# Kernel tuning notes

Measured on AMD Instinct MI355X. Metric: run time of the kernel, lower is better.

Reference implementation:

```python
import jax, jax.numpy as jnp
import numpy as np

H = 4096          # hidden_size
I = 2048          # moe_intermediate_size * n_shared_experts
SWIGLU_LIMIT = 10.0
QMAX = 127.0


def _quantize_weight(w):
    # per-output-channel symmetric int8 quantization of a float weight [out, in]
    s = jnp.maximum(jnp.max(jnp.abs(w), axis=1) / QMAX, 1e-8)      # [out]
    q = jnp.clip(jnp.round(w / s[:, None]), -QMAX, QMAX)           # int8-valued
    return q.astype(jnp.float32), s.astype(jnp.float32)


def setup_inputs() -> dict:
    key = jax.random.key(0)
    ks = jax.random.split(key, 4)
    x = jax.random.normal(ks[0], (2, 4096, H), dtype=jnp.float32)
    w_gate, s_wgate = _quantize_weight(jax.random.normal(ks[1], (I, H)) * 0.02)
    w_up, s_wup = _quantize_weight(jax.random.normal(ks[2], (I, H)) * 0.02)
    w_down, s_wdown = _quantize_weight(jax.random.normal(ks[3], (H, I)) * 0.02)
    inv_gate = jnp.ones((H,), jnp.float32)
    inv_up = jnp.ones((H,), jnp.float32)
    inv_inter = jnp.ones((I,), jnp.float32)
    return {"x": x, "w_gate": w_gate, "s_wgate": s_wgate, "w_up": w_up,
            "s_wup": s_wup, "w_down": w_down, "s_wdown": s_wdown,
            "inv_gate": inv_gate, "inv_up": inv_up, "inv_inter": inv_inter}


def _dynamic_quant(x, inv_smooth):
    # per-token symmetric int8 dynamic quant with smoothing scale
    xs = x.astype(jnp.float32) * inv_smooth                        # [T, D]
    scale = jnp.maximum(jnp.max(jnp.abs(xs), axis=-1, keepdims=True) / QMAX, 1e-8)
    q = jnp.clip(jnp.round(xs / scale), -QMAX, QMAX)
    return q, scale


def _quant_gemm(q, x_scale, w_q, w_scale):
    acc = q @ w_q.T                                                # fp32 accumulate
    return acc * x_scale * w_scale[None, :]


def reference(x, w_gate, s_wgate, w_up, s_wup, w_down, s_wdown,
              inv_gate, inv_up, inv_inter):
    orig_shape = x.shape
    x_flat = x.reshape(-1, H).astype(jnp.bfloat16)                 # [T, H]
    qg, sg = _dynamic_quant(x_flat, inv_gate)
    qu, su = _dynamic_quant(x_flat, inv_up)
    gate_out = _quant_gemm(qg, sg, w_gate, s_wgate)                # [T, I]
    up_out = _quant_gemm(qu, su, w_up, s_wup)                      # [T, I]
    inter = jax.nn.silu(gate_out) * up_out
    inter = jnp.clip(inter, -SWIGLU_LIMIT, SWIGLU_LIMIT).astype(jnp.bfloat16)
    qi, si = _dynamic_quant(inter, inv_inter)
    out = _quant_gemm(qi, si, w_down, s_wdown)                     # [T, H]
    return out.reshape(orig_shape)
```

## Files before the change

kernel.cpp:

```cpp
#include <hip/hip_runtime.h>
#include <hip/hip_bf16.h>


typedef __attribute__((ext_vector_type(4))) int i32x4;

__device__ __forceinline__ void async16(void* lds, const void* g) {
  __builtin_amdgcn_global_load_lds(
      (const __attribute__((address_space(1))) void*)g,
      (__attribute__((address_space(3))) void*)lds, 16, 0, 0);
}

__device__ __forceinline__ i32x4 mfma_i8(i32x4 a, i32x4 b, i32x4 c) {
  return __builtin_amdgcn_mfma_i32_16x16x64_i8(a, b, c, 0, 0, 0);
}

__device__ __forceinline__ float bf16_rne_f(float f) {
  unsigned u = __float_as_uint(f);
  u += 0x7fffu + ((u >> 16) & 1u);
  return __uint_as_float(u & 0xffff0000u);
}

__device__ __forceinline__ unsigned short bf16_bits(float f) {
  unsigned u = __float_as_uint(f);
  u += 0x7fffu + ((u >> 16) & 1u);
  return (unsigned short)(u >> 16);
}

__device__ __forceinline__ float bf16_to_f(unsigned short h) {
  return __uint_as_float(((unsigned)h) << 16);
}

#define BARRIER __builtin_amdgcn_s_barrier()
#define LGKM0 asm volatile("s_waitcnt lgkmcnt(0)" ::: "memory")
#define WAIT_VM8 asm volatile("s_waitcnt vmcnt(8)" ::: "memory")
#define WAIT_VM4 asm volatile("s_waitcnt vmcnt(4)" ::: "memory")
#define WAIT_VM0 asm volatile("s_waitcnt vmcnt(0)" ::: "memory")

__global__ void wconv_kernel(const float* __restrict__ w,
                             signed char* __restrict__ wq, int n) {
  int i = (blockIdx.x * 256 + threadIdx.x) * 4;
  if (i >= n) return;
  float4 f = *(const float4*)(w + i);
  signed char c[4] __attribute__((aligned(4)));
  c[0] = (signed char)(int)rintf(f.x);
  c[1] = (signed char)(int)rintf(f.y);
  c[2] = (signed char)(int)rintf(f.z);
  c[3] = (signed char)(int)rintf(f.w);
  *(int*)(wq + i) = *(const int*)c;
}

__global__ __launch_bounds__(256) void quant_x_kernel(
    const float* __restrict__ x, const float* __restrict__ invg,
    const float* __restrict__ invu, signed char* __restrict__ qg,
    signed char* __restrict__ qu, float* __restrict__ sg,
    float* __restrict__ su, int H) {
  const int t = blockIdx.x, tid = threadIdx.x;
  const float* xr = x + (size_t)t * H;
  const int c0 = tid * 16;
  float xg[16], xu[16];
  float mg = 0.f, mu = 0.f;
#pragma unroll
  for (int v = 0; v < 4; ++v) {
    float4 f = *(const float4*)(xr + c0 + v * 4);
    float4 ig = *(const float4*)(invg + c0 + v * 4);
    float4 iu = *(const float4*)(invu + c0 + v * 4);
    float b0 = bf16_rne_f(f.x), b1 = bf16_rne_f(f.y);
    float b2 = bf16_rne_f(f.z), b3 = bf16_rne_f(f.w);
    xg[v * 4 + 0] = b0 * ig.x; xg[v * 4 + 1] = b1 * ig.y;
    xg[v * 4 + 2] = b2 * ig.z; xg[v * 4 + 3] = b3 * ig.w;
    xu[v * 4 + 0] = b0 * iu.x; xu[v * 4 + 1] = b1 * iu.y;
    xu[v * 4 + 2] = b2 * iu.z; xu[v * 4 + 3] = b3 * iu.w;
#pragma unroll
    for (int j = 0; j < 4; ++j) {
      mg = fmaxf(mg, fabsf(xg[v * 4 + j]));
      mu = fmaxf(mu, fabsf(xu[v * 4 + j]));
    }
  }
#pragma unroll
  for (int off = 32; off > 0; off >>= 1) {
    mg = fmaxf(mg, __shfl_xor(mg, off));
    mu = fmaxf(mu, __shfl_xor(mu, off));
  }
  __shared__ float smg[4], smu[4];
  if ((tid & 63) == 0) { smg[tid >> 6] = mg; smu[tid >> 6] = mu; }
  __syncthreads();
  mg = fmaxf(fmaxf(smg[0], smg[1]), fmaxf(smg[2], smg[3]));
  mu = fmaxf(fmaxf(smu[0], smu[1]), fmaxf(smu[2], smu[3]));
  const float scg = fmaxf(mg / 127.0f, 1e-8f);
  const float scu = fmaxf(mu / 127.0f, 1e-8f);
  signed char og[16] __attribute__((aligned(16)));
  signed char ou[16] __attribute__((aligned(16)));
#pragma unroll
  for (int j = 0; j < 16; ++j) {
    og[j] = (signed char)(int)fminf(fmaxf(rintf(xg[j] / scg), -127.f), 127.f);
    ou[j] = (signed char)(int)fminf(fmaxf(rintf(xu[j] / scu), -127.f), 127.f);
  }
  *(i32x4*)(qg + (size_t)t * H + c0) = *(const i32x4*)og;
  *(i32x4*)(qu + (size_t)t * H + c0) = *(const i32x4*)ou;
  if (tid == 0) { sg[t] = scg; su[t] = scu; }
}

#define G1_STAGE(b, kk)                                                       \
  {                                                                           \
    _Pragma("unroll") for (int p = 0; p < 2; ++p) {                           \
      const int g_ = p * 256 + tid;                                           \
      const int r_ = g_ >> 2;                                                 \
      const int c_ = (g_ & 3) ^ ((r_ >> 1) & 3);                              \
      const size_t ga_ = (size_t)(row0 + r_) * H + (kk) + c_ * 16;            \
      const size_t gb_ = (size_t)(col0 + r_) * H + (kk) + c_ * 16;            \
      async16(&Ag[b][g_ * 16], qg + ga_);                                     \
      async16(&Au[b][g_ * 16], qu + ga_);                                     \
      async16(&Bg[b][g_ * 16], wg + gb_);                                     \
      async16(&Bu[b][g_ * 16], wu + gb_);                                     \
    }                                                                         \
  }

__global__ __launch_bounds__(256, 2) void gemm1_kernel(
    const signed char* __restrict__ qg, const signed char* __restrict__ qu,
    const float* __restrict__ sg, const float* __restrict__ su,
    const signed char* __restrict__ wg, const signed char* __restrict__ wu,
    const float* __restrict__ swg, const float* __restrict__ swu,
    unsigned short* __restrict__ inter, int H, int I) {
  __shared__ signed char Ag[2][128 * 64] __attribute__((aligned(16)));
  __shared__ signed char Au[2][128 * 64] __attribute__((aligned(16)));
  __shared__ signed char Bg[2][128 * 64] __attribute__((aligned(16)));
  __shared__ signed char Bu[2][128 * 64] __attribute__((aligned(16)));
  const int tid = threadIdx.x;
  const int lane = tid & 63, wave = tid >> 6;
  const int row0 = blockIdx.x * 128, col0 = blockIdx.y * 128;
  const int wm = (wave & 1) * 64, wn = (wave >> 1) * 64;
  const int mrow = lane & 15, quad = lane >> 4;
  const int NT = H >> 6;

  int offA[4], offB[4];
#pragma unroll
  for (int i = 0; i < 4; ++i) {
    const int ra = wm + i * 16 + mrow;
    offA[i] = ra * 64 + ((quad ^ ((ra >> 1) & 3)) << 4);
    const int rb = wn + i * 16 + mrow;
    offB[i] = rb * 64 + ((quad ^ ((rb >> 1) & 3)) << 4);
  }

  i32x4 accG[4][4], accU[4][4];
#pragma unroll
  for (int i = 0; i < 4; ++i)
#pragma unroll
    for (int j = 0; j < 4; ++j) {
      accG[i][j] = i32x4{0, 0, 0, 0};
      accU[i][j] = i32x4{0, 0, 0, 0};
    }

  G1_STAGE(0, 0);

  int cur = 0;
  for (int kt = 0; kt < NT; ++kt) {
    if (kt + 1 < NT) {
      G1_STAGE(cur ^ 1, (kt + 1) << 6);
      WAIT_VM8;
    } else {
      WAIT_VM0;
    }
    BARRIER;

    i32x4 aG[4], aU[4], bG[4], bU[4];
#pragma unroll
    for (int i = 0; i < 4; ++i) {
      aG[i] = *(const i32x4*)(&Ag[cur][0] + offA[i]);
      aU[i] = *(const i32x4*)(&Au[cur][0] + offA[i]);
      bG[i] = *(const i32x4*)(&Bg[cur][0] + offB[i]);
      bU[i] = *(const i32x4*)(&Bu[cur][0] + offB[i]);
    }
#pragma unroll
    for (int i = 0; i < 4; ++i)
#pragma unroll
      for (int j = 0; j < 4; ++j) {
        accG[i][j] = mfma_i8(aG[i], bG[j], accG[i][j]);
        accU[i][j] = mfma_i8(aU[i], bU[j], accU[i][j]);
      }

    LGKM0;
    BARRIER;
    cur ^= 1;
  }

  float swgc[4], swuc[4];
#pragma unroll
  for (int j = 0; j < 4; ++j) {
    const int c = col0 + wn + j * 16 + mrow;
    swgc[j] = swg[c];
    swuc[j] = swu[c];
  }
#pragma unroll
  for (int i = 0; i < 4; ++i) {
#pragma unroll
    for (int r = 0; r < 4; ++r) {
      const int row = row0 + wm + i * 16 + quad * 4 + r;
      const float sgr = sg[row], sur = su[row];
#pragma unroll
      for (int j = 0; j < 4; ++j) {
        const int c = col0 + wn + j * 16 + mrow;
        const float g = (float)accG[i][j][r] * sgr * swgc[j];
        const float u = (float)accU[i][j][r] * sur * swuc[j];
        const float sig = 1.f / (1.f + expf(-g));
        float v = (g * sig) * u;
        v = fminf(fmaxf(v, -10.f), 10.f);
        inter[(size_t)row * I + c] = bf16_bits(v);
      }
    }
  }
}

__global__ __launch_bounds__(256) void quant_i_kernel(
    const unsigned short* __restrict__ inter, const float* __restrict__ invi,
    signed char* __restrict__ qi, float* __restrict__ si, int I) {
  const int t = blockIdx.x, tid = threadIdx.x;
  const unsigned short* ir = inter + (size_t)t * I;
  const int c0 = tid * 8;
  uint4 pk = *(const uint4*)(ir + c0);
  float4 i0 = *(const float4*)(invi + c0);
  float4 i1 = *(const float4*)(invi + c0 + 4);
  float xs[8];
  xs[0] = bf16_to_f(pk.x & 0xffffu) * i0.x;
  xs[1] = bf16_to_f(pk.x >> 16) * i0.y;
  xs[2] = bf16_to_f(pk.y & 0xffffu) * i0.z;
  xs[3] = bf16_to_f(pk.y >> 16) * i0.w;
  xs[4] = bf16_to_f(pk.z & 0xffffu) * i1.x;
  xs[5] = bf16_to_f(pk.z >> 16) * i1.y;
  xs[6] = bf16_to_f(pk.w & 0xffffu) * i1.z;
  xs[7] = bf16_to_f(pk.w >> 16) * i1.w;
  float m = 0.f;
#pragma unroll
  for (int j = 0; j < 8; ++j) m = fmaxf(m, fabsf(xs[j]));
#pragma unroll
  for (int off = 32; off > 0; off >>= 1) m = fmaxf(m, __shfl_xor(m, off));
  __shared__ float sm[4];
  if ((tid & 63) == 0) sm[tid >> 6] = m;
  __syncthreads();
  m = fmaxf(fmaxf(sm[0], sm[1]), fmaxf(sm[2], sm[3]));
  const float s = fmaxf(m / 127.0f, 1e-8f);
  signed char o[8] __attribute__((aligned(8)));
#pragma unroll
  for (int j = 0; j < 8; ++j)
    o[j] = (signed char)(int)fminf(fmaxf(rintf(xs[j] / s), -127.f), 127.f);
  *(unsigned long long*)(qi + (size_t)t * I + c0) = *(const unsigned long long*)o;
  if (tid == 0) si[t] = s;
}

#define G2_STAGE(b, kk)                                                       \
  {                                                                           \
    _Pragma("unroll") for (int p = 0; p < 2; ++p) {                           \
      const int g_ = p * 256 + tid;                                           \
      const int r_ = g_ >> 2;                                                 \
      const int c_ = (g_ & 3) ^ ((r_ >> 1) & 3);                              \
      async16(&As[b][g_ * 16],                                                \
              qi + (size_t)(row0 + r_) * I + (kk) + c_ * 16);                 \
      async16(&Bs[b][g_ * 16],                                                \
              wd + (size_t)(col0 + r_) * I + (kk) + c_ * 16);                 \
    }                                                                         \
  }

__global__ __launch_bounds__(256, 2) void gemm2_kernel(
    const signed char* __restrict__ qi, const float* __restrict__ si,
    const signed char* __restrict__ wd, const float* __restrict__ swd,
    float* __restrict__ out, int H, int I) {
  __shared__ signed char As[2][128 * 64] __attribute__((aligned(16)));
  __shared__ signed char Bs[2][128 * 64] __attribute__((aligned(16)));
  const int tid = threadIdx.x;
  const int lane = tid & 63, wave = tid >> 6;
  const int row0 = blockIdx.x * 128, col0 = blockIdx.y * 128;
  const int wm = (wave & 1) * 64, wn = (wave >> 1) * 64;
  const int mrow = lane & 15, quad = lane >> 4;
  const int NT = I >> 6;

  int offA[4], offB[4];
#pragma unroll
  for (int i = 0; i < 4; ++i) {
    const int ra = wm + i * 16 + mrow;
    offA[i] = ra * 64 + ((quad ^ ((ra >> 1) & 3)) << 4);
    const int rb = wn + i * 16 + mrow;
    offB[i] = rb * 64 + ((quad ^ ((rb >> 1) & 3)) << 4);
  }

  i32x4 acc[4][4];
#pragma unroll
  for (int i = 0; i < 4; ++i)
#pragma unroll
    for (int j = 0; j < 4; ++j) acc[i][j] = i32x4{0, 0, 0, 0};

  G2_STAGE(0, 0);

  int cur = 0;
  for (int kt = 0; kt < NT; ++kt) {
    if (kt + 1 < NT) {
      G2_STAGE(cur ^ 1, (kt + 1) << 6);
      WAIT_VM4;
    } else {
      WAIT_VM0;
    }
    BARRIER;

    i32x4 a[4], b[4];
#pragma unroll
    for (int i = 0; i < 4; ++i) {
      a[i] = *(const i32x4*)(&As[cur][0] + offA[i]);
      b[i] = *(const i32x4*)(&Bs[cur][0] + offB[i]);
    }
#pragma unroll
    for (int i = 0; i < 4; ++i)
#pragma unroll
      for (int j = 0; j < 4; ++j) acc[i][j] = mfma_i8(a[i], b[j], acc[i][j]);

    LGKM0;
    BARRIER;
    cur ^= 1;
  }

  float swc[4];
#pragma unroll
  for (int j = 0; j < 4; ++j) swc[j] = swd[col0 + wn + j * 16 + mrow];
#pragma unroll
  for (int i = 0; i < 4; ++i) {
#pragma unroll
    for (int r = 0; r < 4; ++r) {
      const int row = row0 + wm + i * 16 + quad * 4 + r;
      const float sir = si[row];
#pragma unroll
      for (int j = 0; j < 4; ++j) {
        const int c = col0 + wn + j * 16 + mrow;
        out[(size_t)row * H + c] = (float)acc[i][j][r] * sir * swc[j];
      }
    }
  }
}

extern "C" void kernel_launch(void* const* d_in, const int* in_sizes, int n_in,
                              void* d_out, int out_size, void* d_ws,
                              size_t ws_size, hipStream_t stream) {
  const float* x = (const float*)d_in[0];
  const float* w_gate = (const float*)d_in[1];
  const float* s_wgate = (const float*)d_in[2];
  const float* w_up = (const float*)d_in[3];
  const float* s_wup = (const float*)d_in[4];
  const float* w_down = (const float*)d_in[5];
  const float* s_wdown = (const float*)d_in[6];
  const float* inv_gate = (const float*)d_in[7];
  const float* inv_up = (const float*)d_in[8];
  const float* inv_inter = (const float*)d_in[9];
  float* out = (float*)d_out;

  const int H = in_sizes[6];
  const int I = in_sizes[2];
  const int T = in_sizes[0] / H;

  char* ws = (char*)d_ws;
  size_t off = 0;
  signed char* wqg = (signed char*)(ws + off); off += (size_t)I * H;
  signed char* wqu = (signed char*)(ws + off); off += (size_t)I * H;
  signed char* wqd = (signed char*)(ws + off); off += (size_t)H * I;
  signed char* qg  = (signed char*)(ws + off); off += (size_t)T * H;
  signed char* qu  = (signed char*)(ws + off); off += (size_t)T * H;
  unsigned short* inter = (unsigned short*)(ws + off); off += (size_t)T * I * 2;
  float* sg = (float*)(ws + off); off += (size_t)T * 4;
  float* su = (float*)(ws + off); off += (size_t)T * 4;
  float* si = (float*)(ws + off); off += (size_t)T * 4;
  signed char* qi = qg;

  const int nW = I * H;
  wconv_kernel<<<nW / 1024, 256, 0, stream>>>(w_gate, wqg, nW);
  wconv_kernel<<<nW / 1024, 256, 0, stream>>>(w_up, wqu, nW);
  wconv_kernel<<<nW / 1024, 256, 0, stream>>>(w_down, wqd, nW);

  quant_x_kernel<<<T, 256, 0, stream>>>(x, inv_gate, inv_up, qg, qu, sg, su, H);

  dim3 g1(T / 128, I / 128);
  gemm1_kernel<<<g1, 256, 0, stream>>>(qg, qu, sg, su, wqg, wqu, s_wgate,
                                       s_wup, inter, H, I);

  quant_i_kernel<<<T, 256, 0, stream>>>(inter, inv_inter, qi, si, I);

  dim3 g2(T / 128, H / 128);
  gemm2_kernel<<<g2, 256, 0, stream>>>(qi, si, wqd, s_wdown, out, H, I);
}
```

Before: 612.1 us.

## Load weight operands directly from global into registers, bypassing LDS

Both GEMM kernels stop staging the weight (B) tiles through shared memory and instead have each lane read its B fragments straight from global memory into registers at the start of every K-step. Only the activation tiles still go through double-buffered LDS, and the vmcnt waits are lowered to match the smaller async load count. This halves LDS footprint and LDS traffic and may allow higher occupancy. In exchange, weight tiles are re-read per wave from global/L2 without sharing across waves in the block, and the loads are issued in the same iteration they are consumed, so their latency is exposed rather than prefetched.

```diff
diff --git a/kernel.cpp b/kernel.cpp
--- a/kernel.cpp
+++ b/kernel.cpp
@@ -32,8 +32,8 @@
 
 #define BARRIER __builtin_amdgcn_s_barrier()
 #define LGKM0 asm volatile("s_waitcnt lgkmcnt(0)" ::: "memory")
-#define WAIT_VM8 asm volatile("s_waitcnt vmcnt(8)" ::: "memory")
 #define WAIT_VM4 asm volatile("s_waitcnt vmcnt(4)" ::: "memory")
+#define WAIT_VM2 asm volatile("s_waitcnt vmcnt(2)" ::: "memory")
 #define WAIT_VM0 asm volatile("s_waitcnt vmcnt(0)" ::: "memory")
 
 __global__ void wconv_kernel(const float* __restrict__ w,
@@ -107,11 +107,8 @@
       const int r_ = g_ >> 2;                                                 \
       const int c_ = (g_ & 3) ^ ((r_ >> 1) & 3);                              \
       const size_t ga_ = (size_t)(row0 + r_) * H + (kk) + c_ * 16;            \
-      const size_t gb_ = (size_t)(col0 + r_) * H + (kk) + c_ * 16;            \
       async16(&Ag[b][g_ * 16], qg + ga_);                                     \
       async16(&Au[b][g_ * 16], qu + ga_);                                     \
-      async16(&Bg[b][g_ * 16], wg + gb_);                                     \
-      async16(&Bu[b][g_ * 16], wu + gb_);                                     \
     }                                                                         \
   }
 
@@ -123,8 +120,6 @@
     unsigned short* __restrict__ inter, int H, int I) {
   __shared__ signed char Ag[2][128 * 64] __attribute__((aligned(16)));
   __shared__ signed char Au[2][128 * 64] __attribute__((aligned(16)));
-  __shared__ signed char Bg[2][128 * 64] __attribute__((aligned(16)));
-  __shared__ signed char Bu[2][128 * 64] __attribute__((aligned(16)));
   const int tid = threadIdx.x;
   const int lane = tid & 63, wave = tid >> 6;
   const int row0 = blockIdx.x * 128, col0 = blockIdx.y * 128;
@@ -132,14 +127,15 @@
   const int mrow = lane & 15, quad = lane >> 4;
   const int NT = H >> 6;
 
-  int offA[4], offB[4];
+  int offA[4];
 #pragma unroll
   for (int i = 0; i < 4; ++i) {
     const int ra = wm + i * 16 + mrow;
     offA[i] = ra * 64 + ((quad ^ ((ra >> 1) & 3)) << 4);
-    const int rb = wn + i * 16 + mrow;
-    offB[i] = rb * 64 + ((quad ^ ((rb >> 1) & 3)) << 4);
-  }
+  }
+  const size_t jstep = (size_t)16 * H;
+  const signed char* wgB = wg + (size_t)(col0 + wn + mrow) * H + quad * 16;
+  const signed char* wuB = wu + (size_t)(col0 + wn + mrow) * H + quad * 16;
 
   i32x4 accG[4][4], accU[4][4];
 #pragma unroll
@@ -154,21 +150,28 @@
 
   int cur = 0;
   for (int kt = 0; kt < NT; ++kt) {
+    const int kk = kt << 6;
+
+    i32x4 bG[4], bU[4];
+#pragma unroll
+    for (int j = 0; j < 4; ++j) {
+      bG[j] = *(const i32x4*)(wgB + (size_t)j * jstep + kk);
+      bU[j] = *(const i32x4*)(wuB + (size_t)j * jstep + kk);
+    }
+
     if (kt + 1 < NT) {
-      G1_STAGE(cur ^ 1, (kt + 1) << 6);
-      WAIT_VM8;
+      G1_STAGE(cur ^ 1, kk + 64);
+      WAIT_VM4;
     } else {
       WAIT_VM0;
     }
     BARRIER;
 
-    i32x4 aG[4], aU[4], bG[4], bU[4];
+    i32x4 aG[4], aU[4];
 #pragma unroll
     for (int i = 0; i < 4; ++i) {
       aG[i] = *(const i32x4*)(&Ag[cur][0] + offA[i]);
       aU[i] = *(const i32x4*)(&Au[cur][0] + offA[i]);
-      bG[i] = *(const i32x4*)(&Bg[cur][0] + offB[i]);
-      bU[i] = *(const i32x4*)(&Bu[cur][0] + offB[i]);
     }
 #pragma unroll
     for (int i = 0; i < 4; ++i)
@@ -254,8 +257,6 @@
       const int c_ = (g_ & 3) ^ ((r_ >> 1) & 3);                              \
       async16(&As[b][g_ * 16],                                                \
               qi + (size_t)(row0 + r_) * I + (kk) + c_ * 16);                 \
-      async16(&Bs[b][g_ * 16],                                                \
-              wd + (size_t)(col0 + r_) * I + (kk) + c_ * 16);                 \
     }                                                                         \
   }
 
@@ -264,7 +265,6 @@
     const signed char* __restrict__ wd, const float* __restrict__ swd,
     float* __restrict__ out, int H, int I) {
   __shared__ signed char As[2][128 * 64] __attribute__((aligned(16)));
-  __shared__ signed char Bs[2][128 * 64] __attribute__((aligned(16)));
   const int tid = threadIdx.x;
   const int lane = tid & 63, wave = tid >> 6;
   const int row0 = blockIdx.x * 128, col0 = blockIdx.y * 128;
@@ -272,14 +272,14 @@
   const int mrow = lane & 15, quad = lane >> 4;
   const int NT = I >> 6;
 
-  int offA[4], offB[4];
+  int offA[4];
 #pragma unroll
   for (int i = 0; i < 4; ++i) {
     const int ra = wm + i * 16 + mrow;
     offA[i] = ra * 64 + ((quad ^ ((ra >> 1) & 3)) << 4);
-    const int rb = wn + i * 16 + mrow;
-    offB[i] = rb * 64 + ((quad ^ ((rb >> 1) & 3)) << 4);
-  }
+  }
+  const size_t jstep = (size_t)16 * I;
+  const signed char* wdB = wd + (size_t)(col0 + wn + mrow) * I + quad * 16;
 
   i32x4 acc[4][4];
 #pragma unroll
@@ -291,20 +291,25 @@
 
   int cur = 0;
   for (int kt = 0; kt < NT; ++kt) {
+    const int kk = kt << 6;
+
+    i32x4 b[4];
+#pragma unroll
+    for (int j = 0; j < 4; ++j)
+      b[j] = *(const i32x4*)(wdB + (size_t)j * jstep + kk);
+
     if (kt + 1 < NT) {
-      G2_STAGE(cur ^ 1, (kt + 1) << 6);
-      WAIT_VM4;
+      G2_STAGE(cur ^ 1, kk + 64);
+      WAIT_VM2;
     } else {
       WAIT_VM0;
     }
     BARRIER;
 
-    i32x4 a[4], b[4];
-#pragma unroll
-    for (int i = 0; i < 4; ++i) {
+    i32x4 a[4];
+#pragma unroll
+    for (int i = 0; i < 4; ++i)
       a[i] = *(const i32x4*)(&As[cur][0] + offA[i]);
-      b[i] = *(const i32x4*)(&Bs[cur][0] + offB[i]);
-    }
 #pragma unroll
     for (int i = 0; i < 4; ++i)
 #pragma unroll
```

New measurement: 775.1 us. 26.6% more time.
